# Performance work log

Measured on AMD Instinct MI355X. Metric: run time of the kernel, lower is better.

## Reference

```python
import jax, jax.numpy as jnp
import numpy as np

LATENT = 512
N_VARS = 8
IN_DIM = N_VARS + 1            # x concat dt
MOTOR = int(0.3 * LATENT)      # 153 (AutoNCP output_size)
_IC = LATENT - MOTOR           # 359
COMMAND = max(int(0.4 * _IC), 1)  # 143
INTER = _IC - COMMAND          # 216
B, T = 128, 256


def _build_masks(seed=22222, density=0.5):
    """Faithful numpy port of ncps AutoNCP/NCP wiring build (seed 22222).
    Returns the three binary sparsity masks used by WiredCfCCell, each of
    shape (out, in) = abs(concat([inter_layer_adjacency, ones(hh)], 0).T)."""
    rng = np.random.RandomState(seed)
    motor_ids = list(range(MOTOR))
    command_ids = list(range(MOTOR, MOTOR + COMMAND))
    inter_ids = list(range(MOTOR + COMMAND, LATENT))
    sensory_ids = list(range(IN_DIM))
    s_fanout = max(int(INTER * density), 1)
    i_fanout = max(int(COMMAND * density), 1)
    rec = max(int(COMMAND * density * 2), 1)
    m_fanin = max(int(COMMAND * density), 1)
    adj = np.zeros((LATENT, LATENT), np.float32)
    sadj = np.zeros((IN_DIM, LATENT), np.float32)
    # sensory -> inter
    unreach = list(inter_ids)
    for src in sensory_ids:
        for dest in rng.choice(inter_ids, size=s_fanout, replace=False):
            if dest in unreach:
                unreach.remove(dest)
            sadj[src, dest] = rng.choice([-1, 1])
    fanin = int(np.clip(int(IN_DIM * s_fanout / INTER), 1, IN_DIM))
    for dest in unreach:
        for src in rng.choice(sensory_ids, size=fanin, replace=False):
            sadj[src, dest] = rng.choice([-1, 1])
    # inter -> command
    unreach = list(command_ids)
    for src in inter_ids:
        for dest in rng.choice(command_ids, size=i_fanout, replace=False):
            if dest in unreach:
                unreach.remove(dest)
            adj[src, dest] = rng.choice([-1, 1])
    fanin = int(np.clip(int(INTER * i_fanout / COMMAND), 1, COMMAND))
    for dest in unreach:
        for src in rng.choice(inter_ids, size=fanin, replace=False):
            adj[src, dest] = rng.choice([-1, 1])
    # recurrent command synapses
    for _ in range(rec):
        adj[rng.choice(command_ids), rng.choice(command_ids)] = rng.choice([-1, 1])
    # command -> motor
    unreach = list(command_ids)
    for dest in motor_ids:
        for src in rng.choice(command_ids, size=m_fanin, replace=False):
            if src in unreach:
                unreach.remove(src)
            adj[src, dest] = rng.choice([-1, 1])
    fanout = int(np.clip(int(MOTOR * m_fanin / COMMAND), 1, MOTOR))
    for src in unreach:
        for dest in rng.choice(motor_ids, size=fanout, replace=False):
            adj[src, dest] = rng.choice([-1, 1])
    m0 = np.concatenate([sadj[:, inter_ids], np.ones((INTER, INTER), np.float32)], 0)
    m1 = np.concatenate([adj[np.ix_(inter_ids, command_ids)], np.ones((COMMAND, COMMAND), np.float32)], 0)
    m2 = np.concatenate([adj[np.ix_(command_ids, motor_ids)], np.ones((MOTOR, MOTOR), np.float32)], 0)
    return [np.abs(m.T).astype(np.int32) for m in (m0, m1, m2)]


def setup_inputs() -> dict:
    key = jax.random.key(0)
    ks = jax.random.split(key, 40)

    def lin(k, out_d, in_d):
        return (jax.random.normal(k, (out_d, in_d), jnp.float32) / np.sqrt(in_d)).astype(jnp.float32)

    m0, m1, m2 = _build_masks()
    dims = [(INTER, IN_DIM + INTER), (COMMAND, INTER + COMMAND), (MOTOR, COMMAND + MOTOR)]
    inp = {
        "x": jax.random.normal(ks[0], (B, T, N_VARS), jnp.float32),
        "dt": jax.random.uniform(ks[1], (B, T, 1), jnp.float32),
        "lstm_wi": lin(ks[2], 4 * LATENT, IN_DIM),
        "lstm_wr": lin(ks[3], 4 * LATENT, LATENT),
        "lstm_bi": jnp.zeros((4 * LATENT,), jnp.float32),
    }
    i = 4
    for l, (o, d) in enumerate(dims):
        for nm in ("w1", "w2", "wa", "wb"):
            inp[f"{nm}_{l}"] = lin(ks[i], o, d)
            i += 1
            inp[f"b{nm[1]}_{l}"] = jnp.zeros((o,), jnp.float32)
    inp["m0"] = jnp.asarray(m0)
    inp["m1"] = jnp.asarray(m1)
    inp["m2"] = jnp.asarray(m2)
    return inp


def _forward(x, dt, lstm_wi, lstm_wr, lstm_bi, layers, masks):
    seq = jnp.concatenate([x, dt], -1).transpose(1, 0, 2)  # (T, B, IN_DIM)

    def cfc_layer(params, mask, inp, hl):
        # CfCCell, mode=default, no backbone, sparsity on ff1/ff2, ts = 1.0
        w1, b1, w2, b2, wa, ba, wb, bb = params
        xc = jnp.concatenate([inp, hl], -1)
        ff1 = jnp.tanh(xc @ (w1 * mask).T + b1)
        ff2 = jnp.tanh(xc @ (w2 * mask).T + b2)
        ti = jax.nn.sigmoid(-(xc @ wa.T + ba) + (xc @ wb.T + bb))
        return ff1 * (1.0 - ti) + ti * ff2

    def step(carry, xt):
        h, c = carry
        # ncps LSTMCell (mixed memory), forget-gate bias +1
        z = xt @ lstm_wi.T + lstm_bi + h @ lstm_wr.T
        i, ig, fg, og = jnp.split(z, 4, axis=-1)
        c = c * jax.nn.sigmoid(fg + 1.0) + jnp.tanh(i) * jax.nn.sigmoid(ig)
        h = jnp.tanh(c) * jax.nn.sigmoid(og)
        # WiredCfCCell: 3 layers (inter, command, motor), sequential
        hs = (h[:, :INTER], h[:, INTER:INTER + COMMAND], h[:, INTER + COMMAND:])
        inp, new_hs = xt, []
        for p, m, hl in zip(layers, masks, hs):
            inp = cfc_layer(p, m, inp, hl)
            new_hs.append(inp)
        return (jnp.concatenate(new_hs, -1), c), None

    h0 = jnp.zeros((x.shape[0], LATENT), jnp.float32)
    (h, c), _ = jax.lax.scan(step, (h0, h0), seq)
    return h, c


def reference(x, dt, lstm_wi, lstm_wr, lstm_bi,
              w1_0, b1_0, w2_0, b2_0, wa_0, ba_0, wb_0, bb_0,
              w1_1, b1_1, w2_1, b2_1, wa_1, ba_1, wb_1, bb_1,
              w1_2, b1_2, w2_2, b2_2, wa_2, ba_2, wb_2, bb_2,
              m0, m1, m2):
    layers = [
        (w1_0, b1_0, w2_0, b2_0, wa_0, ba_0, wb_0, bb_0),
        (w1_1, b1_1, w2_1, b2_1, wa_1, ba_1, wb_1, bb_1),
        (w1_2, b1_2, w2_2, b2_2, wa_2, ba_2, wb_2, bb_2),
    ]
    masks = [m.astype(jnp.float32) for m in (m0, m1, m2)]
    h, c = _forward(x, dt, lstm_wi, lstm_wr, lstm_bi, layers, masks)
    return h, c
```

## Files before the change

kernel.cpp:

```cpp
#include <hip/hip_runtime.h>
#include <stdint.h>

typedef unsigned int u32;
typedef unsigned short u16;

#define TT 256

#define LSW 272
#define OFF_L0  (2048*LSW)
#define OFF_L1  (OFF_L0 + 864*128)
#define OFF_L2  (OFF_L1 + 576*192)
#define OFF_HL  (OFF_L2 + 640*160)
#define OFF_REC (OFF_HL + 128*264)
#define OFF_SYNC (OFF_REC + 128*264)
#define WS_TOTAL (OFF_SYNC + 4096)
#define NFL 16

__device__ __forceinline__ u16 f2bf(float f){
  u32 u = __builtin_bit_cast(u32, f);
  u += 0x7FFFu + ((u >> 16) & 1u);
  return (u16)(u >> 16);
}
__device__ __forceinline__ u32 packbf(float lo, float hi){
  return (u32)f2bf(lo) | ((u32)f2bf(hi) << 16);
}
__device__ __forceinline__ float bdot(u32 a, u32 b, float c){
  float d;
  asm("v_dot2_f32_bf16 %0, %1, %2, %3" : "=v"(d) : "v"(a), "v"(b), "v"(c));
  return d;
}
__device__ __forceinline__ float sigm(float x){ return 1.0f/(1.0f + __expf(-x)); }
__device__ __forceinline__ float tanh_(float x){ return 1.0f - 2.0f/(1.0f + __expf(2.0f*x)); }

__device__ __forceinline__ u32 xload(const u32* p){
  return __hip_atomic_load(p, __ATOMIC_RELAXED, __HIP_MEMORY_SCOPE_AGENT);
}
__device__ __forceinline__ void xstore16(u16* p, u16 v){
  __hip_atomic_store(p, v, __ATOMIC_RELAXED, __HIP_MEMORY_SCOPE_AGENT);
}

__device__ __forceinline__ void bar_arrive(u32* fl, int s, u32 v){
  __syncthreads();
  if (threadIdx.x == 0)
    __hip_atomic_store(&fl[s*NFL], v, __ATOMIC_RELAXED, __HIP_MEMORY_SCOPE_AGENT);
}
__device__ __forceinline__ void bar_wait(const u32* fl, u32 v){
  if (threadIdx.x < 8){
    int guard = 1 << 16;
    while (__hip_atomic_load(&fl[threadIdx.x*NFL], __ATOMIC_RELAXED, __HIP_MEMORY_SCOPE_AGENT) < v
           && --guard) __builtin_amdgcn_s_sleep(1);
  }
  __syncthreads();
  asm volatile("" ::: "memory");
}

__device__ __forceinline__ float lstmval(const float* wi, const float* wr, int r, int s){
  if (s < 9)  return wi[r*9 + s];
  if (s == 9 || s == 369 || s >= 523) return 0.f;
  if (s < 369) return wr[r*512 + s - 10];
  return wr[r*512 + s - 11];
}
__device__ __forceinline__ float l0val(const float* W, const int* M, int o, int k){
  if (k == 9 || k >= 226) return 0.f;
  int ki = (k < 9) ? k : k - 1;
  float w = W[o*225 + ki];
  if (M) w *= (float)M[o*225 + ki];
  return w;
}
__device__ __forceinline__ float l1val(const float* W, const int* M, int o, int k){
  if (k >= 359) return 0.f;
  float w = W[o*359 + k];
  if (M) w *= (float)M[o*359 + k];
  return w;
}
__device__ __forceinline__ float l2val(const float* W, const int* M, int o, int k){
  if (k == 143 || k == 144 || k >= 298) return 0.f;
  int ki = (k < 143) ? k : k - 2;
  float w = W[o*296 + ki];
  if (M) w *= (float)M[o*296 + ki];
  return w;
}

__global__ void prep_kernel(
    const float* __restrict__ wi, const float* __restrict__ wr,
    const float* __restrict__ w10,const float* __restrict__ w20,const float* __restrict__ wa0,const float* __restrict__ wb0,const int* __restrict__ m0,
    const float* __restrict__ w11,const float* __restrict__ w21,const float* __restrict__ wa1,const float* __restrict__ wb1,const int* __restrict__ m1,
    const float* __restrict__ w12,const float* __restrict__ w22,const float* __restrict__ wa2,const float* __restrict__ wb2,const int* __restrict__ m2,
    u32* __restrict__ ws)
{
  for (int i = blockIdx.x*blockDim.x + threadIdx.x; i < WS_TOTAL; i += gridDim.x*blockDim.x){
    float lo = 0.f, hi = 0.f;
    if (i < OFF_L0){
      int row = i / LSW, k2 = i - row*LSW;
      int orig = (row >> 2) + ((row & 3) << 9);
      lo = lstmval(wi, wr, orig, 2*k2);
      hi = lstmval(wi, wr, orig, 2*k2+1);
    } else if (i < OFF_L1){
      int loc = i - OFF_L0;
      int row = loc >> 7, k2 = loc & 127;
      int o = row >> 2, m = row & 3;
      const float* W = (m==0)?w10:(m==1)?w20:(m==2)?wa0:wb0;
      const int* M = (m < 2) ? m0 : nullptr;
      lo = l0val(W, M, o, 2*k2); hi = l0val(W, M, o, 2*k2+1);
    } else if (i < OFF_L2){
      int loc = i - OFF_L1;
      int row = loc / 192, k2 = loc - row*192;
      int o = row >> 2, m = row & 3;
      if (o < 143){
        const float* W = (m==0)?w11:(m==1)?w21:(m==2)?wa1:wb1;
        const int* M = (m < 2) ? m1 : nullptr;
        lo = l1val(W, M, o, 2*k2); hi = l1val(W, M, o, 2*k2+1);
      }
    } else if (i < OFF_HL){
      int loc = i - OFF_L2;
      int row = loc / 160, k2 = loc - row*160;
      int o = row >> 2, m = row & 3;
      if (o < 153){
        const float* W = (m==0)?w12:(m==1)?w22:(m==2)?wa2:wb2;
        const int* M = (m < 2) ? m2 : nullptr;
        lo = l2val(W, M, o, 2*k2); hi = l2val(W, M, o, 2*k2+1);
      }
    } else {
      ws[i] = 0u;
      continue;
    }
    ws[i] = packbf(lo, hi);
  }
}

__global__ __launch_bounds__(1024) void liquid_rnn(
    const float* __restrict__ x, const float* __restrict__ dtp,
    const float* __restrict__ lstm_bi,
    const float* __restrict__ b10, const float* __restrict__ b20,
    const float* __restrict__ ba0, const float* __restrict__ bb0,
    const float* __restrict__ b11, const float* __restrict__ b21,
    const float* __restrict__ ba1, const float* __restrict__ bb1,
    const float* __restrict__ b12, const float* __restrict__ b22,
    const float* __restrict__ ba2, const float* __restrict__ bb2,
    u32* __restrict__ ws, float* __restrict__ out)
{
  __shared__ u32 xcS[4][272];

  const int tid  = threadIdx.x;
  const int bid  = blockIdx.x;
  const int s    = bid & 7;
  const int quad = bid >> 3;
  const int b4   = tid & 3;
  const int rr   = tid >> 2;
  const int batch= quad*4 + b4;

  u32* hlw  = ws + OFF_HL;
  u32* recw = ws + OFF_REC;
  u16* hl16 = (u16*)hlw;
  u16* rec16= (u16*)recw;
  u32* fl   = ws + OFF_SYNC + quad*(8*NFL);

  const int vA = s*64 + (rr >> 2);
  const float lb = lstm_bi[vA + 512*(rr & 3)];
  int oB = 0; float biasB = 0.f;
  if (tid < 432){ int m = rr & 3; oB = 27*s + (rr >> 2);
    biasB = ((m==0)?b10:(m==1)?b20:(m==2)?ba0:bb0)[oB]; }
  int oC = 0; float biasC = 0.f;
  if (tid < 288){ int m = rr & 3; oC = 18*s + (rr >> 2);
    if (oC < 143) biasC = ((m==0)?b11:(m==1)?b21:(m==2)?ba1:bb1)[oC]; }
  int oD = 0; float biasD = 0.f;
  if (tid < 320){ int m = rr & 3; oD = 20*s + (rr >> 2);
    if (oD < 153) biasD = ((m==0)?b12:(m==1)?b22:(m==2)?ba2:bb2)[oD]; }

  for (int i = tid; i < 4*272; i += 1024) ((u32*)xcS)[i] = 0u;
  float creg = 0.f;
  __syncthreads();

  for (int t = 0; t < TT; ++t){
    const u32 vb = 4u*(u32)t;
    if (tid < 20){
      int bb = tid/5, w = tid - bb*5;
      int bg = quad*4 + bb;
      float e0, e1;
      if (w < 4){ e0 = x[((size_t)bg*TT + t)*8 + 2*w]; e1 = x[((size_t)bg*TT + t)*8 + 2*w+1]; }
      else      { e0 = dtp[(size_t)bg*TT + t]; e1 = 0.f; }
      xcS[bb][w] = packbf(e0, e1);
    }
    if (tid < 720){
      int bb = tid/180, j = tid - bb*180;
      xcS[bb][5+j] = xload(&recw[(size_t)(quad*4+bb)*264 + j]);
    }
    bar_wait(fl, vb);
    { int bb = tid >> 8, w = tid & 255;
      if (w >= 180) xcS[bb][5+w] = xload(&recw[(size_t)(quad*4+bb)*264 + w]); }
    if (tid < 4) xcS[tid][261] = xload(&recw[(size_t)(quad*4+tid)*264 + 256]);
    __syncthreads();
    {
      float A = lb;
      const u32* wrow = ws + (size_t)(s*256 + rr)*LSW;
      #pragma unroll 4
      for (int g = 0; g < 68; ++g){
        uint4 wv = *(const uint4*)(wrow + (g<<2));
        uint4 av = *(const uint4*)&xcS[b4][g<<2];
        A = bdot(wv.x, av.x, A); A = bdot(wv.y, av.y, A);
        A = bdot(wv.z, av.z, A); A = bdot(wv.w, av.w, A);
      }
      float zig = __shfl_down(A, 4), zfg = __shfl_down(A, 8), zog = __shfl_down(A, 12);
      if (!(rr & 3)){
        creg = creg * sigm(zfg + 1.0f) + tanh_(A) * sigm(zig);
        float hl = tanh_(creg) * sigm(zog);
        xstore16(&hl16[(size_t)batch*528 + vA], f2bf(hl));
      }
    }
    bar_arrive(fl, s, vb+1);  bar_wait(fl, vb+1);
    if (tid < 432){ int bb = tid/108, j = tid - bb*108;
      xcS[bb][5+j] = xload(&hlw[(size_t)(quad*4+bb)*264 + j]); }
    __syncthreads();
    if (tid < 432){
      float A = biasB;
      const u32* wrow = ws + OFF_L0 + (size_t)(s*108 + rr)*128;
      #pragma unroll 2
      for (int g = 0; g < 30; ++g){
        uint4 wv = *(const uint4*)(wrow + (g<<2));
        uint4 av = *(const uint4*)&xcS[b4][g<<2];
        A = bdot(wv.x, av.x, A); A = bdot(wv.y, av.y, A);
        A = bdot(wv.z, av.z, A); A = bdot(wv.w, av.w, A);
      }
      float A1 = __shfl_down(A, 4), A2 = __shfl_down(A, 8), A3 = __shfl_down(A, 12);
      if (!(rr & 3)){
        float ti = sigm(A3 - A2);
        float o0 = tanh_(A)*(1.f - ti) + ti*tanh_(A1);
        xstore16(&rec16[(size_t)batch*528 + oB], f2bf(o0));
        if (t == TT-1) out[(size_t)batch*512 + oB] = o0;
      }
    }
    bar_arrive(fl, s, vb+2);  bar_wait(fl, vb+2);
    if (tid < 720){ int bb = tid/180, j = tid - bb*180;
      u32 v = (j < 108) ? xload(&recw[(size_t)(quad*4+bb)*264 + j])
                        : xload(&hlw[(size_t)(quad*4+bb)*264 + j]);
      xcS[bb][j] = v; }
    __syncthreads();
    if (tid < 288){
      float A = biasC;
      const u32* wrow = ws + OFF_L1 + (size_t)(s*72 + rr)*192;
      #pragma unroll 4
      for (int g = 0; g < 48; ++g){
        uint4 wv = *(const uint4*)(wrow + (g<<2));
        uint4 av = *(const uint4*)&xcS[b4][g<<2];
        A = bdot(wv.x, av.x, A); A = bdot(wv.y, av.y, A);
        A = bdot(wv.z, av.z, A); A = bdot(wv.w, av.w, A);
      }
      float A1 = __shfl_down(A, 4), A2 = __shfl_down(A, 8), A3 = __shfl_down(A, 12);
      if (!(rr & 3) && oC < 143){
        float ti = sigm(A3 - A2);
        float o0 = tanh_(A)*(1.f - ti) + ti*tanh_(A1);
        xstore16(&rec16[(size_t)batch*528 + 216 + oC], f2bf(o0));
        if (t == TT-1) out[(size_t)batch*512 + 216 + oC] = o0;
      }
    }
    bar_arrive(fl, s, vb+3);  bar_wait(fl, vb+3);
    if (tid < 596){ int bb = tid/149, j = tid - bb*149;
      u32 v;
      if (j < 72)      v = xload(&recw[(size_t)(quad*4+bb)*264 + 108 + j]);
      else if (j == 72) v = xload(&hlw[(size_t)(quad*4+bb)*264 + 179]);
      else              v = xload(&hlw[(size_t)(quad*4+bb)*264 + 180 + (j-73)]);
      xcS[bb][j] = v; }
    __syncthreads();
    if (tid < 320){
      float A = biasD;
      const u32* wrow = ws + OFF_L2 + (size_t)(s*80 + rr)*160;
      #pragma unroll 4
      for (int g = 0; g < 40; ++g){
        uint4 wv = *(const uint4*)(wrow + (g<<2));
        uint4 av = *(const uint4*)&xcS[b4][g<<2];
        A = bdot(wv.x, av.x, A); A = bdot(wv.y, av.y, A);
        A = bdot(wv.z, av.z, A); A = bdot(wv.w, av.w, A);
      }
      float A1 = __shfl_down(A, 4), A2 = __shfl_down(A, 8), A3 = __shfl_down(A, 12);
      if (!(rr & 3) && oD < 153){
        float ti = sigm(A3 - A2);
        float o0 = tanh_(A)*(1.f - ti) + ti*tanh_(A1);
        xstore16(&rec16[(size_t)batch*528 + 360 + oD], f2bf(o0));
        if (t == TT-1) out[(size_t)batch*512 + 359 + oD] = o0;
      }
    }
    bar_arrive(fl, s, vb+4);
  }

  if (!(rr & 3)) out[65536 + (size_t)batch*512 + vA] = creg;
}

extern "C" void kernel_launch(void* const* d_in, const int* in_sizes, int n_in,
                              void* d_out, int out_size, void* d_ws, size_t ws_size,
                              hipStream_t stream)
{
  (void)in_sizes; (void)n_in; (void)out_size; (void)ws_size;
  const float* x   = (const float*)d_in[0];
  const float* dt  = (const float*)d_in[1];
  const float* wi  = (const float*)d_in[2];
  const float* wr  = (const float*)d_in[3];
  const float* bi  = (const float*)d_in[4];
  const float* w10 = (const float*)d_in[5];  const float* b10 = (const float*)d_in[6];
  const float* w20 = (const float*)d_in[7];  const float* b20 = (const float*)d_in[8];
  const float* wa0 = (const float*)d_in[9];  const float* ba0 = (const float*)d_in[10];
  const float* wb0 = (const float*)d_in[11]; const float* bb0 = (const float*)d_in[12];
  const float* w11 = (const float*)d_in[13]; const float* b11 = (const float*)d_in[14];
  const float* w21 = (const float*)d_in[15]; const float* b21 = (const float*)d_in[16];
  const float* wa1 = (const float*)d_in[17]; const float* ba1 = (const float*)d_in[18];
  const float* wb1 = (const float*)d_in[19]; const float* bb1 = (const float*)d_in[20];
  const float* w12 = (const float*)d_in[21]; const float* b12 = (const float*)d_in[22];
  const float* w22 = (const float*)d_in[23]; const float* b22 = (const float*)d_in[24];
  const float* wa2 = (const float*)d_in[25]; const float* ba2 = (const float*)d_in[26];
  const float* wb2 = (const float*)d_in[27]; const float* bb2 = (const float*)d_in[28];
  const int* m0 = (const int*)d_in[29];
  const int* m1 = (const int*)d_in[30];
  const int* m2 = (const int*)d_in[31];

  u32* ws    = (u32*)d_ws;
  float* out = (float*)d_out;

  prep_kernel<<<dim3(931), dim3(1024), 0, stream>>>(
      wi, wr,
      w10,w20,wa0,wb0,m0,
      w11,w21,wa1,wb1,m1,
      w12,w22,wa2,wb2,m2,
      ws);

  liquid_rnn<<<dim3(256), dim3(1024), 0, stream>>>(
      x, dt, bi,
      b10,b20,ba0,bb0,
      b11,b21,ba1,bb1,
      b12,b22,ba2,bb2,
      ws, out);
}
```

Measured before the change: 6.048 ms.

## Software-pipeline recurrent step to overlap partial dot products with cross-block waits

Restructures the per-timestep loop into a skewed pipeline. Each layer's dot product is split into the part that depends on values already available and the part that needs freshly published values, and the first part runs before waiting on the inter-block flag. Weight and activation layouts are repadded (16-aligned input segments, narrower layer-0 rows), and separate shared buffers per layer remove the restaging of one shared vector. The intent is to hide global barrier latency and cut redundant shared-memory reloads, at the cost of more complex flag sequencing and a prologue and epilogue.

```diff
diff --git a/kernel.cpp b/kernel.cpp
--- a/kernel.cpp
+++ b/kernel.cpp
@@ -7,10 +7,13 @@
 #define TT 256
 
 #define LSW 272
+#define B0W 120
+#define C1W 192
+#define D2W 160
 #define OFF_L0  (2048*LSW)
-#define OFF_L1  (OFF_L0 + 864*128)
-#define OFF_L2  (OFF_L1 + 576*192)
-#define OFF_HL  (OFF_L2 + 640*160)
+#define OFF_L1  (OFF_L0 + 864*B0W)
+#define OFF_L2  (OFF_L1 + 576*C1W)
+#define OFF_HL  (OFF_L2 + 640*D2W)
 #define OFF_REC (OFF_HL + 128*264)
 #define OFF_SYNC (OFF_REC + 128*264)
 #define WS_TOTAL (OFF_SYNC + 4096)
@@ -54,15 +57,30 @@
   asm volatile("" ::: "memory");
 }
 
+template<int G0, int G1>
+__device__ __forceinline__ float dotg(const u32* wrow, const u32* xc, float A){
+  #pragma unroll
+  for (int g = G0; g < G1; ++g){
+    uint4 wv = *(const uint4*)(wrow + (g<<2));
+    uint4 av = *(const uint4*)(xc + (g<<2));
+    A=bdot(wv.x,av.x,A); A=bdot(wv.y,av.y,A); A=bdot(wv.z,av.z,A); A=bdot(wv.w,av.w,A);
+  }
+  return A;
+}
+
 __device__ __forceinline__ float lstmval(const float* wi, const float* wr, int r, int s){
-  if (s < 9)  return wi[r*9 + s];
-  if (s == 9 || s == 369 || s >= 523) return 0.f;
-  if (s < 369) return wr[r*512 + s - 10];
-  return wr[r*512 + s - 11];
+  if (s < 9)   return wi[r*9 + s];
+  if (s < 16)  return 0.f;
+  if (s < 375) return wr[r*512 + (s-16)];
+  if (s == 375) return 0.f;
+  if (s < 529) return wr[r*512 + (s-17)];
+  return 0.f;
 }
 __device__ __forceinline__ float l0val(const float* W, const int* M, int o, int k){
-  if (k == 9 || k >= 226) return 0.f;
-  int ki = (k < 9) ? k : k - 1;
+  int ki;
+  if (k < 9) ki = k;
+  else if (k >= 16 && k < 232) ki = 9 + (k - 16);
+  else return 0.f;
   float w = W[o*225 + ki];
   if (M) w *= (float)M[o*225 + ki];
   return w;
@@ -97,14 +115,14 @@
       hi = lstmval(wi, wr, orig, 2*k2+1);
     } else if (i < OFF_L1){
       int loc = i - OFF_L0;
-      int row = loc >> 7, k2 = loc & 127;
+      int row = loc / B0W, k2 = loc - row*B0W;
       int o = row >> 2, m = row & 3;
       const float* W = (m==0)?w10:(m==1)?w20:(m==2)?wa0:wb0;
       const int* M = (m < 2) ? m0 : nullptr;
       lo = l0val(W, M, o, 2*k2); hi = l0val(W, M, o, 2*k2+1);
     } else if (i < OFF_L2){
       int loc = i - OFF_L1;
-      int row = loc / 192, k2 = loc - row*192;
+      int row = loc / C1W, k2 = loc - row*C1W;
       int o = row >> 2, m = row & 3;
       if (o < 143){
         const float* W = (m==0)?w11:(m==1)?w21:(m==2)?wa1:wb1;
@@ -113,7 +131,7 @@
       }
     } else if (i < OFF_HL){
       int loc = i - OFF_L2;
-      int row = loc / 160, k2 = loc - row*160;
+      int row = loc / D2W, k2 = loc - row*D2W;
       int o = row >> 2, m = row & 3;
       if (o < 153){
         const float* W = (m==0)?w12:(m==1)?w22:(m==2)?wa2:wb2;
@@ -139,7 +157,10 @@
     const float* __restrict__ ba2, const float* __restrict__ bb2,
     u32* __restrict__ ws, float* __restrict__ out)
 {
-  __shared__ u32 xcS[4][272];
+  __shared__ u32 xcA[4][272];
+  __shared__ u32 xcB[4][120];
+  __shared__ u32 xcC[4][192];
+  __shared__ u32 xcD[4][160];
 
   const int tid  = threadIdx.x;
   const int bid  = blockIdx.x;
@@ -167,119 +188,156 @@
   if (tid < 320){ int m = rr & 3; oD = 20*s + (rr >> 2);
     if (oD < 153) biasD = ((m==0)?b12:(m==1)?b22:(m==2)?ba2:bb2)[oD]; }
 
-  for (int i = tid; i < 4*272; i += 1024) ((u32*)xcS)[i] = 0u;
+  const u32* wrA = ws + (size_t)(s*256 + rr)*LSW;
+  const u32* wrB = ws + OFF_L0 + (size_t)(s*108 + (rr < 108 ? rr : 0))*B0W;
+  const u32* wrC = ws + OFF_L1 + (size_t)(s*72  + (rr < 72  ? rr : 0))*C1W;
+  const u32* wrD = ws + OFF_L2 + (size_t)(s*80  + (rr < 80  ? rr : 0))*D2W;
+
+  auto stage_xt = [&](u32 (*dst)[272], int tt, int idx){
+    int bb = idx/5, w = idx - bb*5;
+    int bg = quad*4 + bb;
+    float e0, e1;
+    if (w < 4){ e0 = x[((size_t)bg*TT + tt)*8 + 2*w]; e1 = x[((size_t)bg*TT + tt)*8 + 2*w+1]; }
+    else      { e0 = dtp[(size_t)bg*TT + tt]; e1 = 0.f; }
+    dst[bb][w] = packbf(e0, e1);
+  };
+  auto stage_xtB = [&](int tt, int idx){
+    int bb = idx/5, w = idx - bb*5;
+    int bg = quad*4 + bb;
+    float e0, e1;
+    if (w < 4){ e0 = x[((size_t)bg*TT + tt)*8 + 2*w]; e1 = x[((size_t)bg*TT + tt)*8 + 2*w+1]; }
+    else      { e0 = dtp[(size_t)bg*TT + tt]; e1 = 0.f; }
+    xcB[bb][w] = packbf(e0, e1);
+  };
+
+  for (int i = tid; i < 4*272; i += 1024) ((u32*)xcA)[i] = 0u;
+  for (int i = tid; i < 4*120; i += 1024) ((u32*)xcB)[i] = 0u;
+  for (int i = tid; i < 4*192; i += 1024) ((u32*)xcC)[i] = 0u;
+  for (int i = tid; i < 4*160; i += 1024) ((u32*)xcD)[i] = 0u;
   float creg = 0.f;
-  __syncthreads();
-
-  for (int t = 0; t < TT; ++t){
-    const u32 vb = 4u*(u32)t;
-    if (tid < 20){
-      int bb = tid/5, w = tid - bb*5;
-      int bg = quad*4 + bb;
-      float e0, e1;
-      if (w < 4){ e0 = x[((size_t)bg*TT + t)*8 + 2*w]; e1 = x[((size_t)bg*TT + t)*8 + 2*w+1]; }
-      else      { e0 = dtp[(size_t)bg*TT + t]; e1 = 0.f; }
-      xcS[bb][w] = packbf(e0, e1);
-    }
-    if (tid < 720){
-      int bb = tid/180, j = tid - bb*180;
-      xcS[bb][5+j] = xload(&recw[(size_t)(quad*4+bb)*264 + j]);
-    }
-    bar_wait(fl, vb);
-    { int bb = tid >> 8, w = tid & 255;
-      if (w >= 180) xcS[bb][5+w] = xload(&recw[(size_t)(quad*4+bb)*264 + w]); }
-    if (tid < 4) xcS[tid][261] = xload(&recw[(size_t)(quad*4+tid)*264 + 256]);
+  float accA = lb, accC = biasC, accD = biasD;
+  __syncthreads();
+  if (tid < 20){ stage_xt(xcA, 0, tid); stage_xtB(0, tid); }
+  __syncthreads();
+
+  {
+    accA = dotg<0,2>(wrA, xcA[b4], accA);
+    float zig = __shfl_down(accA, 4), zfg = __shfl_down(accA, 8), zog = __shfl_down(accA, 12);
+    if (!(rr & 3)){
+      creg = creg * sigm(zfg + 1.0f) + tanh_(accA) * sigm(zig);
+      float hl = tanh_(creg) * sigm(zog);
+      xstore16(&hl16[(size_t)batch*528 + vA], f2bf(hl));
+    }
+    accA = lb;
+  }
+  bar_arrive(fl, s, 1);
+  bar_wait(fl, 1);
+  {
+    int bb = tid >> 8, w = tid & 255;
+    u32 v = xload(&hlw[(size_t)(quad*4+bb)*264 + w]);
+    if (w < 108) xcB[bb][8+w] = v;
+    else if (w < 180){ xcC[bb][w] = v; if (w == 179) xcD[bb][72] = v; }
+    else xcD[bb][w-107] = v;
+  }
+  __syncthreads();
+  if (tid < 432){
+    float A0 = dotg<0,30>(wrB, xcB[b4], biasB);
+    float A1 = __shfl_down(A0, 4), A2 = __shfl_down(A0, 8), A3 = __shfl_down(A0, 12);
+    if (!(rr & 3)){
+      float ti = sigm(A3 - A2);
+      float o0 = tanh_(A0)*(1.f - ti) + ti*tanh_(A1);
+      xstore16(&rec16[(size_t)batch*528 + oB], f2bf(o0));
+    }
+  }
+  bar_arrive(fl, s, 2);
+  if (tid < 20) stage_xt(xcA, 1, tid);
+
+  for (int k = 0; k < TT; ++k){
+    const u32 fb = 4u*(u32)k;
+    if (tid < 288) accC = dotg<27,48>(wrC, xcC[b4], accC);
+    if (tid < 320) accD = dotg<18,40>(wrD, xcD[b4], accD);
+    bar_wait(fl, fb+2);
+    if (tid < 432){
+      int bb = tid/108, j = tid - bb*108;
+      u32 v = xload(&recw[(size_t)(quad*4+bb)*264 + j]);
+      xcA[bb][8+j] = v; xcC[bb][j] = v;
+    } else if (tid < 452 && k+1 < TT){
+      stage_xtB(k+1, tid-432);
+    }
+    __syncthreads();
+    if (tid < 288){
+      float A0 = dotg<0,27>(wrC, xcC[b4], accC);
+      float A1 = __shfl_down(A0, 4), A2 = __shfl_down(A0, 8), A3 = __shfl_down(A0, 12);
+      if (!(rr & 3) && oC < 143){
+        float ti = sigm(A3 - A2);
+        float o0 = tanh_(A0)*(1.f - ti) + ti*tanh_(A1);
+        xstore16(&rec16[(size_t)batch*528 + 216 + oC], f2bf(o0));
+        if (k == TT-1) out[(size_t)batch*512 + 216 + oC] = o0;
+      }
+      accC = biasC;
+    }
+    bar_arrive(fl, s, fb+3);
+    accA = dotg<0,29>(wrA, xcA[b4], accA);
+    bar_wait(fl, fb+3);
+    if (tid < 288){
+      int bb = tid/72, j = tid - bb*72;
+      u32 v = xload(&recw[(size_t)(quad*4+bb)*264 + 108 + j]);
+      xcA[bb][116+j] = v; xcD[bb][j] = v;
+    }
+    __syncthreads();
+    if (tid < 320){
+      float A0 = dotg<0,18>(wrD, xcD[b4], accD);
+      float A1 = __shfl_down(A0, 4), A2 = __shfl_down(A0, 8), A3 = __shfl_down(A0, 12);
+      if (!(rr & 3) && oD < 153){
+        float ti = sigm(A3 - A2);
+        float o0 = tanh_(A0)*(1.f - ti) + ti*tanh_(A1);
+        xstore16(&rec16[(size_t)batch*528 + 360 + oD], f2bf(o0));
+        if (k == TT-1) out[(size_t)batch*512 + 359 + oD] = o0;
+      }
+      accD = biasD;
+    }
+    bar_arrive(fl, s, fb+4);
+    if (k == TT-1) break;
+    accA = dotg<29,47>(wrA, xcA[b4], accA);
+    bar_wait(fl, fb+4);
+    if (tid < 308){
+      int bb = tid/77, j = tid - bb*77;
+      xcA[bb][188+j] = xload(&recw[(size_t)(quad*4+bb)*264 + 180 + j]);
+    } else if (tid < 328 && k+2 < TT){
+      stage_xt(xcA, k+2, tid-308);
+    }
     __syncthreads();
     {
-      float A = lb;
-      const u32* wrow = ws + (size_t)(s*256 + rr)*LSW;
-      #pragma unroll 4
-      for (int g = 0; g < 68; ++g){
-        uint4 wv = *(const uint4*)(wrow + (g<<2));
-        uint4 av = *(const uint4*)&xcS[b4][g<<2];
-        A = bdot(wv.x, av.x, A); A = bdot(wv.y, av.y, A);
-        A = bdot(wv.z, av.z, A); A = bdot(wv.w, av.w, A);
-      }
-      float zig = __shfl_down(A, 4), zfg = __shfl_down(A, 8), zog = __shfl_down(A, 12);
+      accA = dotg<47,67>(wrA, xcA[b4], accA);
+      float zig = __shfl_down(accA, 4), zfg = __shfl_down(accA, 8), zog = __shfl_down(accA, 12);
       if (!(rr & 3)){
-        creg = creg * sigm(zfg + 1.0f) + tanh_(A) * sigm(zig);
+        creg = creg * sigm(zfg + 1.0f) + tanh_(accA) * sigm(zig);
         float hl = tanh_(creg) * sigm(zog);
         xstore16(&hl16[(size_t)batch*528 + vA], f2bf(hl));
       }
-    }
-    bar_arrive(fl, s, vb+1);  bar_wait(fl, vb+1);
-    if (tid < 432){ int bb = tid/108, j = tid - bb*108;
-      xcS[bb][5+j] = xload(&hlw[(size_t)(quad*4+bb)*264 + j]); }
+      accA = lb;
+    }
+    bar_arrive(fl, s, fb+5);
+    bar_wait(fl, fb+5);
+    {
+      int bb = tid >> 8, w = tid & 255;
+      u32 v = xload(&hlw[(size_t)(quad*4+bb)*264 + w]);
+      if (w < 108) xcB[bb][8+w] = v;
+      else if (w < 180){ xcC[bb][w] = v; if (w == 179) xcD[bb][72] = v; }
+      else xcD[bb][w-107] = v;
+    }
     __syncthreads();
     if (tid < 432){
-      float A = biasB;
-      const u32* wrow = ws + OFF_L0 + (size_t)(s*108 + rr)*128;
-      #pragma unroll 2
-      for (int g = 0; g < 30; ++g){
-        uint4 wv = *(const uint4*)(wrow + (g<<2));
-        uint4 av = *(const uint4*)&xcS[b4][g<<2];
-        A = bdot(wv.x, av.x, A); A = bdot(wv.y, av.y, A);
-        A = bdot(wv.z, av.z, A); A = bdot(wv.w, av.w, A);
-      }
-      float A1 = __shfl_down(A, 4), A2 = __shfl_down(A, 8), A3 = __shfl_down(A, 12);
+      float A0 = dotg<0,30>(wrB, xcB[b4], biasB);
+      float A1 = __shfl_down(A0, 4), A2 = __shfl_down(A0, 8), A3 = __shfl_down(A0, 12);
       if (!(rr & 3)){
         float ti = sigm(A3 - A2);
-        float o0 = tanh_(A)*(1.f - ti) + ti*tanh_(A1);
+        float o0 = tanh_(A0)*(1.f - ti) + ti*tanh_(A1);
         xstore16(&rec16[(size_t)batch*528 + oB], f2bf(o0));
-        if (t == TT-1) out[(size_t)batch*512 + oB] = o0;
-      }
-    }
-    bar_arrive(fl, s, vb+2);  bar_wait(fl, vb+2);
-    if (tid < 720){ int bb = tid/180, j = tid - bb*180;
-      u32 v = (j < 108) ? xload(&recw[(size_t)(quad*4+bb)*264 + j])
-                        : xload(&hlw[(size_t)(quad*4+bb)*264 + j]);
-      xcS[bb][j] = v; }
-    __syncthreads();
-    if (tid < 288){
-      float A = biasC;
-      const u32* wrow = ws + OFF_L1 + (size_t)(s*72 + rr)*192;
-      #pragma unroll 4
-      for (int g = 0; g < 48; ++g){
-        uint4 wv = *(const uint4*)(wrow + (g<<2));
-        uint4 av = *(const uint4*)&xcS[b4][g<<2];
-        A = bdot(wv.x, av.x, A); A = bdot(wv.y, av.y, A);
-        A = bdot(wv.z, av.z, A); A = bdot(wv.w, av.w, A);
-      }
-      float A1 = __shfl_down(A, 4), A2 = __shfl_down(A, 8), A3 = __shfl_down(A, 12);
-      if (!(rr & 3) && oC < 143){
-        float ti = sigm(A3 - A2);
-        float o0 = tanh_(A)*(1.f - ti) + ti*tanh_(A1);
-        xstore16(&rec16[(size_t)batch*528 + 216 + oC], f2bf(o0));
-        if (t == TT-1) out[(size_t)batch*512 + 216 + oC] = o0;
-      }
-    }
-    bar_arrive(fl, s, vb+3);  bar_wait(fl, vb+3);
-    if (tid < 596){ int bb = tid/149, j = tid - bb*149;
-      u32 v;
-      if (j < 72)      v = xload(&recw[(size_t)(quad*4+bb)*264 + 108 + j]);
-      else if (j == 72) v = xload(&hlw[(size_t)(quad*4+bb)*264 + 179]);
-      else              v = xload(&hlw[(size_t)(quad*4+bb)*264 + 180 + (j-73)]);
-      xcS[bb][j] = v; }
-    __syncthreads();
-    if (tid < 320){
-      float A = biasD;
-      const u32* wrow = ws + OFF_L2 + (size_t)(s*80 + rr)*160;
-      #pragma unroll 4
-      for (int g = 0; g < 40; ++g){
-        uint4 wv = *(const uint4*)(wrow + (g<<2));
-        uint4 av = *(const uint4*)&xcS[b4][g<<2];
-        A = bdot(wv.x, av.x, A); A = bdot(wv.y, av.y, A);
-        A = bdot(wv.z, av.z, A); A = bdot(wv.w, av.w, A);
-      }
-      float A1 = __shfl_down(A, 4), A2 = __shfl_down(A, 8), A3 = __shfl_down(A, 12);
-      if (!(rr & 3) && oD < 153){
-        float ti = sigm(A3 - A2);
-        float o0 = tanh_(A)*(1.f - ti) + ti*tanh_(A1);
-        xstore16(&rec16[(size_t)batch*528 + 360 + oD], f2bf(o0));
-        if (t == TT-1) out[(size_t)batch*512 + 359 + oD] = o0;
-      }
-    }
-    bar_arrive(fl, s, vb+4);
+        if (k+1 == TT-1) out[(size_t)batch*512 + oB] = o0;
+      }
+    }
+    bar_arrive(fl, s, fb+6);
   }
 
   if (!(rr & 3)) out[65536 + (size_t)batch*512 + vA] = creg;
@@ -314,7 +372,7 @@
   u32* ws    = (u32*)d_ws;
   float* out = (float*)d_out;
 
-  prep_kernel<<<dim3(931), dim3(1024), 0, stream>>>(
+  prep_kernel<<<dim3(924), dim3(1024), 0, stream>>>(
       wi, wr,
       w10,w20,wa0,wb0,m0,
       w11,w21,wa1,wb1,m1,
```

Result: no change. 6.093 ms (+0.7%).

## Compute motor layer redundantly per block to drop one grid barrier per step

Applied to the files above, without the earlier changes.

Every block now computes all motor-layer outputs for its four batches locally, with four gate accumulators per thread, and keeps them in a shared buffer. The next step's LSTM input reads that buffer instead of fetching motor state from global memory written by other blocks. This removes one cross-block barrier wait and arrive per timestep, so the barrier counter now advances by three per step instead of four. In exchange each block repeats motor-layer work that other blocks also do, and every block writes the same final motor outputs.

```diff
diff --git a/kernel.cpp b/kernel.cpp
--- a/kernel.cpp
+++ b/kernel.cpp
@@ -140,6 +140,7 @@
     u32* __restrict__ ws, float* __restrict__ out)
 {
   __shared__ u32 xcS[4][272];
+  __shared__ u32 i2l[4][78];
 
   const int tid  = threadIdx.x;
   const int bid  = blockIdx.x;
@@ -163,16 +164,16 @@
   int oC = 0; float biasC = 0.f;
   if (tid < 288){ int m = rr & 3; oC = 18*s + (rr >> 2);
     if (oC < 143) biasC = ((m==0)?b11:(m==1)?b21:(m==2)?ba1:bb1)[oC]; }
-  int oD = 0; float biasD = 0.f;
-  if (tid < 320){ int m = rr & 3; oD = 20*s + (rr >> 2);
-    if (oD < 153) biasD = ((m==0)?b12:(m==1)?b22:(m==2)?ba2:bb2)[oD]; }
+  float bD1=0,bD2=0,bDa=0,bDb=0;
+  if (rr < 153){ bD1=b12[rr]; bD2=b22[rr]; bDa=ba2[rr]; bDb=bb2[rr]; }
 
   for (int i = tid; i < 4*272; i += 1024) ((u32*)xcS)[i] = 0u;
+  for (int i = tid; i < 4*78;  i += 1024) ((u32*)i2l)[i] = 0u;
   float creg = 0.f;
   __syncthreads();
 
   for (int t = 0; t < TT; ++t){
-    const u32 vb = 4u*(u32)t;
+    const u32 vb = 3u*(u32)t;
     if (tid < 20){
       int bb = tid/5, w = tid - bb*5;
       int bg = quad*4 + bb;
@@ -185,10 +186,10 @@
       int bb = tid/180, j = tid - bb*180;
       xcS[bb][5+j] = xload(&recw[(size_t)(quad*4+bb)*264 + j]);
     }
-    bar_wait(fl, vb);
-    { int bb = tid >> 8, w = tid & 255;
-      if (w >= 180) xcS[bb][5+w] = xload(&recw[(size_t)(quad*4+bb)*264 + w]); }
-    if (tid < 4) xcS[tid][261] = xload(&recw[(size_t)(quad*4+tid)*264 + 256]);
+    if (tid < 308){
+      int bb = tid/77, k = tid - bb*77;
+      xcS[bb][185+k] = i2l[bb][k];
+    }
     __syncthreads();
     {
       float A = lb;
@@ -261,25 +262,27 @@
       else              v = xload(&hlw[(size_t)(quad*4+bb)*264 + 180 + (j-73)]);
       xcS[bb][j] = v; }
     __syncthreads();
-    if (tid < 320){
-      float A = biasD;
-      const u32* wrow = ws + OFF_L2 + (size_t)(s*80 + rr)*160;
+    if (tid < 612){
+      float A0=bD1, A1=bD2, A2=bDa, A3=bDb;
+      const u32* p = ws + OFF_L2 + (size_t)(4*rr)*160;
       #pragma unroll 4
       for (int g = 0; g < 40; ++g){
-        uint4 wv = *(const uint4*)(wrow + (g<<2));
         uint4 av = *(const uint4*)&xcS[b4][g<<2];
-        A = bdot(wv.x, av.x, A); A = bdot(wv.y, av.y, A);
-        A = bdot(wv.z, av.z, A); A = bdot(wv.w, av.w, A);
-      }
-      float A1 = __shfl_down(A, 4), A2 = __shfl_down(A, 8), A3 = __shfl_down(A, 12);
-      if (!(rr & 3) && oD < 153){
-        float ti = sigm(A3 - A2);
-        float o0 = tanh_(A)*(1.f - ti) + ti*tanh_(A1);
-        xstore16(&rec16[(size_t)batch*528 + 360 + oD], f2bf(o0));
-        if (t == TT-1) out[(size_t)batch*512 + 359 + oD] = o0;
-      }
-    }
-    bar_arrive(fl, s, vb+4);
+        uint4 w0 = *(const uint4*)(p + (g<<2));
+        uint4 w1 = *(const uint4*)(p + 160 + (g<<2));
+        uint4 w2 = *(const uint4*)(p + 320 + (g<<2));
+        uint4 w3 = *(const uint4*)(p + 480 + (g<<2));
+        A0=bdot(w0.x,av.x,A0); A0=bdot(w0.y,av.y,A0); A0=bdot(w0.z,av.z,A0); A0=bdot(w0.w,av.w,A0);
+        A1=bdot(w1.x,av.x,A1); A1=bdot(w1.y,av.y,A1); A1=bdot(w1.z,av.z,A1); A1=bdot(w1.w,av.w,A1);
+        A2=bdot(w2.x,av.x,A2); A2=bdot(w2.y,av.y,A2); A2=bdot(w2.z,av.z,A2); A2=bdot(w2.w,av.w,A2);
+        A3=bdot(w3.x,av.x,A3); A3=bdot(w3.y,av.y,A3); A3=bdot(w3.z,av.z,A3); A3=bdot(w3.w,av.w,A3);
+      }
+      float ti = sigm(A3 - A2);
+      float o0 = tanh_(A0)*(1.f - ti) + ti*tanh_(A1);
+      ((u16*)i2l[b4])[rr] = f2bf(o0);
+      if (t == TT-1) out[(size_t)batch*512 + 359 + rr] = o0;
+    }
+    __syncthreads();
   }
 
   if (!(rr & 3)) out[65536 + (size_t)batch*512 + vA] = creg;
```

After: 9.239 ms. 52.8% more time.
